# Kernel optimization log

Measured on AMD Instinct MI355X. Metric: run time of the kernel, lower is better.

The kernel has to match this reference:

```python
import jax, jax.numpy as jnp
import numpy as np

N = 4096        # num nodes
D = 512         # d_model (in_dim)
F = 512         # dff (out_dim)
H = 4           # num_heads
ALPHA = 0.3     # tf.keras LeakyReLU default


def setup_inputs() -> dict:
    key = jax.random.key(0)
    ks = jax.random.split(key, 9)
    s_in = 1.0 / np.sqrt(D)
    s_out = 1.0 / np.sqrt(F)
    return {
        "nodes": jax.random.normal(ks[0], (N, D), jnp.float32),
        "edges": jax.random.normal(ks[1], (N, D), jnp.float32),
        "labels": jax.random.normal(ks[2], (N, D), jnp.float32),
        # edge_layer Dense(dff)
        "We": jax.random.normal(ks[3], (D, F), jnp.float32) * s_in,
        "be": jnp.zeros((F,), jnp.float32),
        # per-head kernels stacked on leading head axis
        "W": jax.random.normal(ks[4], (H, D, F), jnp.float32) * s_in,
        "b": jax.random.normal(ks[5], (H, F), jnp.float32) * 0.01,
        "u": jax.random.normal(ks[6], (H, F), jnp.float32) * s_out,  # attn_kernel_self (squeezed)
        "v": jax.random.normal(ks[7], (H, F), jnp.float32) * s_out,  # attn_kernel_neighs (squeezed)
    }


def reference(nodes, edges, labels, We, be, W, b, u, v):
    # edge projection shared across heads: Dense(edges + labels)
    e = (edges + labels) @ We + be                       # [N, F]
    # per-head node projection: features = nodes @ W_h + b_h
    feats = jnp.einsum('nd,hdf->hnf', nodes, W) + b[:, None, :]   # [H, N, F]
    # rank-1 additive attention scores
    a_self = jnp.einsum('hnf,hf->hn', feats, u)          # [H, N]
    a_neigh = jnp.einsum('hnf,hf->hn', feats, v)         # [H, N]
    feats = feats + e[None]                              # [H, N, F]
    scores = a_self[:, :, None] * a_neigh[:, None, :]    # [H, N, N] outer product
    scores = jnp.where(scores >= 0, scores, ALPHA * scores)  # LeakyReLU(0.3)
    attn = jax.nn.softmax(scores, axis=-1)               # [H, N, N]
    out = jnp.einsum('hnm,hmf->hnf', attn, feats)        # [H, N, F]
    return jax.nn.relu(out.mean(axis=0))                 # [N, F]
```

## Files before the change

kernel.cpp:

```cpp
#include <hip/hip_runtime.h>

#define NN 4096
#define DD 512
#define FF 512
#define HH 4
#define KK 1024

typedef _Float16 f16;
typedef f16 f16x8 __attribute__((ext_vector_type(8)));
typedef f16 f16x4 __attribute__((ext_vector_type(4)));
typedef float f32x4 __attribute__((ext_vector_type(4)));
typedef float f32x16 __attribute__((ext_vector_type(16)));

typedef __attribute__((address_space(1))) void gvoid;
typedef __attribute__((address_space(3))) void svoid;
__device__ __forceinline__ void glds16(const void* g, void* s) {
    __builtin_amdgcn_global_load_lds((gvoid*)g, (svoid*)s, 16, 0, 0);
}

__device__ __attribute__((aligned(16))) f16 g_catA[NN * KK];
__device__ __attribute__((aligned(16))) f16 g_catB[HH * FF * KK];
__device__ __attribute__((aligned(16))) f16 g_featsH[HH * FF * NN];
__device__ __attribute__((aligned(16))) f16 g_oaccH[(size_t)2 * HH * NN * FF];
__device__ float g_Zp[2 * HH * NN];
__device__ float g_bcat[HH * FF];
__device__ float g_tu[HH * DD], g_tv[HH * DD], g_bu[HH], g_bv[HH];
__device__ float g_p[HH * NN], g_q[HH * NN], g_M[HH * NN];

#define PREP_CONV 4104
#define PREP_TRAN 320
#define PREP_UV   513

__global__ __launch_bounds__(256) void k_prep(const float* __restrict__ nodes, const float* __restrict__ edges,
                                              const float* __restrict__ labels, const float* __restrict__ We,
                                              const float* __restrict__ W, const float* __restrict__ be,
                                              const float* __restrict__ b, const float* __restrict__ u,
                                              const float* __restrict__ v) {
    __shared__ float lds[64 * 65];
    int bx = blockIdx.x;
    int tid = threadIdx.x;
    if (bx < PREP_CONV) {
        int id = bx * 256 + tid;
        const int NQ = NN * DD / 4;
        if (id < NQ) {
            f32x4 vv = *(const f32x4*)(nodes + (size_t)id * 4);
            f16x4 ov;
#pragma unroll
            for (int k = 0; k < 4; ++k) ov[k] = (f16)vv[k];
            *(f16x4*)&g_catA[(size_t)(id >> 7) * KK + (id & 127) * 4] = ov;
            return;
        }
        id -= NQ;
        if (id < NQ) {
            f32x4 ev = *(const f32x4*)(edges  + (size_t)id * 4);
            f32x4 lv = *(const f32x4*)(labels + (size_t)id * 4);
            f16x4 ov;
#pragma unroll
            for (int k = 0; k < 4; ++k) ov[k] = (f16)(ev[k] + lv[k]);
            *(f16x4*)&g_catA[(size_t)(id >> 7) * KK + 512 + (id & 127) * 4] = ov;
            return;
        }
        id -= NQ;
        if (id < HH * FF) { g_bcat[id] = b[id] + be[id & 511]; return; }
        return;
    }
    if (bx < PREP_CONV + PREP_TRAN) {
        int bid = bx - PREP_CONV;
        int mi = bid >> 6;
        int t64 = bid & 63;
        const float* src = (mi == 0) ? We : (W + (size_t)(mi - 1) * DD * FF);
        int ti = t64 >> 3, tj = t64 & 7;
        int r = tid >> 2, cseg = (tid & 3) * 16;
#pragma unroll
        for (int kq = 0; kq < 4; ++kq) {
            f32x4 vv = *(const f32x4*)(src + (size_t)(ti * 64 + r) * 512 + tj * 64 + cseg + kq * 4);
            *(f32x4*)&lds[r * 65 + cseg + kq * 4] = vv;
        }
        __syncthreads();
        int fl = tid >> 2, dseg = (tid & 3) * 16;
        f16x8 o0, o1;
#pragma unroll
        for (int k = 0; k < 8; ++k) o0[k] = (f16)lds[(dseg + k) * 65 + fl];
#pragma unroll
        for (int k = 0; k < 8; ++k) o1[k] = (f16)lds[(dseg + 8 + k) * 65 + fl];
        size_t frow = (size_t)(tj * 64 + fl);
        size_t dcol = (size_t)(ti * 64 + dseg);
        if (mi == 0) {
#pragma unroll
            for (int hh = 0; hh < HH; ++hh) {
                size_t ob = ((size_t)hh * FF + frow) * KK + 512 + dcol;
                *(f16x8*)&g_catB[ob] = o0;
                *(f16x8*)&g_catB[ob + 8] = o1;
            }
        } else {
            size_t ob = ((size_t)(mi - 1) * FF + frow) * KK + dcol;
            *(f16x8*)&g_catB[ob] = o0;
            *(f16x8*)&g_catB[ob + 8] = o1;
        }
        return;
    }
    {
        int row = (bx - PREP_CONV - PREP_TRAN) * 4 + (tid >> 6);
        int lane = tid & 63;
        float su = 0.f, sv = 0.f;
        if (row < HH * DD) {
            int h = row >> 9, d = row & 511;
            size_t wb = (size_t)h * DD * FF + (size_t)d * FF;
#pragma unroll
            for (int j = 0; j < 8; ++j) {
                int f = lane + 64 * j;
                float wv = W[wb + f];
                su += wv * u[(size_t)h * FF + f];
                sv += wv * v[(size_t)h * FF + f];
            }
        } else if (row < HH * DD + HH) {
            int h = row - HH * DD;
#pragma unroll
            for (int j = 0; j < 8; ++j) {
                int f = lane + 64 * j;
                float bvv = b[(size_t)h * FF + f];
                su += bvv * u[(size_t)h * FF + f];
                sv += bvv * v[(size_t)h * FF + f];
            }
        }
#pragma unroll
        for (int m = 1; m < 64; m <<= 1) {
            su += __shfl_xor(su, m, 64);
            sv += __shfl_xor(sv, m, 64);
        }
        if (lane == 0 && row < HH * DD + HH) {
            if (row < HH * DD) { g_tu[row] = su; g_tv[row] = sv; }
            else { g_bu[row - HH * DD] = su; g_bv[row - HH * DD] = sv; }
        }
    }
}

__global__ __launch_bounds__(256) void k_pq() {
    int row = blockIdx.x * 4 + (threadIdx.x >> 6);
    int lane = threadIdx.x & 63;
    int h = row >> 12, n = row & 4095;
    const f16* nb = g_catA + (size_t)n * KK + lane * 8;
    const float* tu = g_tu + h * DD + lane * 8;
    const float* tv = g_tv + h * DD + lane * 8;
    f16x8 nv8 = *(const f16x8*)nb;
    f32x4 tu0 = *(const f32x4*)tu, tu1 = *(const f32x4*)(tu + 4);
    f32x4 tv0 = *(const f32x4*)tv, tv1 = *(const f32x4*)(tv + 4);
    float pa = 0.f, qa = 0.f;
#pragma unroll
    for (int j = 0; j < 4; ++j) {
        float nv = (float)nv8[j];
        pa += nv * tu0[j];
        qa += nv * tv0[j];
    }
#pragma unroll
    for (int j = 0; j < 4; ++j) {
        float nv = (float)nv8[4 + j];
        pa += nv * tu1[j];
        qa += nv * tv1[j];
    }
#pragma unroll
    for (int m = 1; m < 64; m <<= 1) {
        pa += __shfl_xor(pa, m, 64);
        qa += __shfl_xor(qa, m, 64);
    }
    if (lane == 0) {
        g_p[row] = pa + g_bu[h];
        g_q[row] = qa + g_bv[h];
    }
}

__global__ __launch_bounds__(256, 2) void k_gemm_feats() {
    __shared__ f16 As[128 * 128];
    __shared__ f16 Bs[128 * 128];
    int tid = threadIdx.x;
    int lane = tid & 63, wave = tid >> 6;
    int wr = wave & 1, wc = wave >> 1;
    int c = lane & 15, g = lane >> 4;
    int n0 = blockIdx.x * 128, f0 = blockIdx.y * 128;
    int h = blockIdx.z;
    const f16* Bgl = g_catB + (size_t)h * FF * KK;
    int r4 = lane >> 4;
    int ch = lane & 15;
    f32x4 acc[4][4] = {};
    for (int kk = 0; kk < KK; kk += 128) {
        __syncthreads();
#pragma unroll
        for (int j = 0; j < 8; ++j) {
            int rowb = wave * 32 + j * 4;
            int row = rowb + r4;
            int src = (ch ^ (row & 15)) * 8;
            glds16(g_catA + (size_t)(n0 + row) * KK + kk + src, &As[rowb * 128]);
            glds16(Bgl    + (size_t)(f0 + row) * KK + kk + src, &Bs[rowb * 128]);
        }
        __syncthreads();
#pragma unroll
        for (int s = 0; s < 4; ++s) {
            f16x8 af[4], bf[4];
#pragma unroll
            for (int i = 0; i < 4; ++i) {
                int ra = wr * 64 + i * 16 + c;
                af[i] = *(const f16x8*)&As[ra * 128 + (((s * 4 + g) ^ (ra & 15)) * 8)];
            }
#pragma unroll
            for (int jj = 0; jj < 4; ++jj) {
                int rb = wc * 64 + jj * 16 + c;
                bf[jj] = *(const f16x8*)&Bs[rb * 128 + (((s * 4 + g) ^ (rb & 15)) * 8)];
            }
#pragma unroll
            for (int i = 0; i < 4; ++i)
#pragma unroll
                for (int jj = 0; jj < 4; ++jj)
                    acc[i][jj] = __builtin_amdgcn_mfma_f32_16x16x32_f16(af[i], bf[jj], acc[i][jj], 0, 0, 0);
        }
    }
#pragma unroll
    for (int jj = 0; jj < 4; ++jj) {
        int f = f0 + wc * 64 + jj * 16 + c;
        float bv = g_bcat[h * FF + f];
#pragma unroll
        for (int i = 0; i < 4; ++i) {
            int r0 = n0 + wr * 64 + i * 16 + g * 4;
            f16x4 ov;
#pragma unroll
            for (int rr = 0; rr < 4; ++rr) ov[rr] = (f16)(acc[i][jj][rr] + bv);
            *(f16x4*)(g_featsH + ((size_t)h * FF + f) * NN + r0) = ov;
        }
    }
}

__global__ __launch_bounds__(256) void k_mstat() {
    __shared__ float red[256];
    int h = blockIdx.x;
    int tid = threadIdx.x;
    float lmax = -1e30f, lmin = 1e30f;
    for (int i = tid; i < NN; i += 256) {
        float qv = g_q[h * NN + i];
        lmax = fmaxf(lmax, qv);
        lmin = fminf(lmin, qv);
    }
    red[tid] = lmax;
    __syncthreads();
    for (int s = 128; s > 0; s >>= 1) {
        if (tid < s) red[tid] = fmaxf(red[tid], red[tid + s]);
        __syncthreads();
    }
    float qmax = red[0];
    __syncthreads();
    red[tid] = lmin;
    __syncthreads();
    for (int s = 128; s > 0; s >>= 1) {
        if (tid < s) red[tid] = fminf(red[tid], red[tid + s]);
        __syncthreads();
    }
    float qmin = red[0];
#pragma unroll
    for (int j = 0; j < 16; ++j) {
        int n = tid + j * 256;
        float pv = g_p[h * NN + n];
        float se = pv * (pv >= 0.f ? qmax : qmin);
        g_M[h * NN + n] = fmaxf(se, 0.3f * se);
    }
}

#define WCALC(qv, dstvec, idx)                                              \
    {                                                                       \
        float s_ = pv * (qv);                                               \
        s_ = fmaxf(s_, 0.3f * s_);                                          \
        float e_ = __builtin_amdgcn_exp2f(__builtin_fmaf(s_, L2E, -mvb));   \
        zacc += e_;                                                         \
        dstvec[idx] = (f16)e_;                                              \
    }
#define GEN8(qa, qb, w)                                                     \
    {                                                                       \
        _Pragma("unroll") for (int k_ = 0; k_ < 4; ++k_) {                  \
            WCALC((qa)[k_], w, k_);                                         \
            WCALC((qb)[k_], w, 4 + k_);                                     \
        }                                                                   \
    }
#define STAGE_B(buf, kkoff)                                                 \
    {                                                                       \
        _Pragma("unroll") for (int j = 0; j < 8; ++j) {                     \
            int row_ = wave * 64 + j * 8 + r8;                              \
            glds16(Bgl + (size_t)row_ * NN + (kkoff) + ((ch ^ (row_ & 7)) * 8), \
                   &Bs[buf][(wave * 64 + j * 8) * 64]);                     \
        }                                                                   \
    }

__global__ __launch_bounds__(512, 2) void k_gemm_out() {
    __shared__ f16 As2[2][128 * 64];
    __shared__ f16 Bs[2][512 * 64];
    int tid = threadIdx.x;
    int lane = tid & 63, wave = tid >> 6;
    int wr = wave & 1;
    int wf = wave >> 1;
    int c5 = lane & 31, h5 = lane >> 5;
    int n0 = blockIdx.x * 128;
    int h = blockIdx.y;
    int ks = blockIdx.z;
    int wn = tid >> 2, kq = (tid & 3) * 16;
    const float L2E = 1.44269504f;
    float pv = g_p[h * NN + n0 + wn];
    float mvb = g_M[h * NN + n0 + wn] * L2E + 6.0f;
    const float* qh = g_q + h * NN + ks * 2048;
    const f16* Bgl = g_featsH + (size_t)h * FF * NN + (size_t)ks * 2048;
    int r8 = lane >> 3, ch = lane & 7;
    int aw0 = wn * 64 + (((tid & 3) * 2 + 0) ^ (wn & 7)) * 8;
    int aw1 = wn * 64 + (((tid & 3) * 2 + 1) ^ (wn & 7)) * 8;
    int arow = (wr * 64 + c5) * 64;
    int brow = (wf * 128 + c5) * 64;
    int csw = (c5 & 7);
    float zacc = 0.f;
    f32x16 acc[2][4] = {};
    f16x8 wA, wB;

    {
        const float* qp = qh + kq;
        f32x4 q0 = *(const f32x4*)qp, q1 = *(const f32x4*)(qp + 4),
              q2 = *(const f32x4*)(qp + 8), q3 = *(const f32x4*)(qp + 12);
        GEN8(q0, q1, wA);
        GEN8(q2, q3, wB);
        *(f16x8*)&As2[0][aw0] = wA;
        *(f16x8*)&As2[0][aw1] = wB;
        STAGE_B(0, 0);
        const float* qp1 = qh + 64 + kq;
        q0 = *(const f32x4*)qp1; q1 = *(const f32x4*)(qp1 + 4);
        q2 = *(const f32x4*)(qp1 + 8); q3 = *(const f32x4*)(qp1 + 12);
        GEN8(q0, q1, wA);
        GEN8(q2, q3, wB);
    }
    __syncthreads();

    int cur = 0;
    for (int t = 0; t < 32; ++t) {
        f32x4 q0, q1, q2, q3;
        if (t < 30) {
            const float* qp = qh + t * 64 + 128 + kq;
            q0 = *(const f32x4*)qp; q1 = *(const f32x4*)(qp + 4);
            q2 = *(const f32x4*)(qp + 8); q3 = *(const f32x4*)(qp + 12);
        }
        if (t < 31) {
            int nxt = cur ^ 1;
            int kk2 = t * 64 + 64;
            STAGE_B(nxt, kk2);
            *(f16x8*)&As2[nxt][aw0] = wA;
            *(f16x8*)&As2[nxt][aw1] = wB;
        }
#pragma unroll
        for (int sk = 0; sk < 4; ++sk) {
            int cph = ((sk * 2 + h5) ^ csw) * 8;
            f16x8 af0 = *(const f16x8*)&As2[cur][arow + cph];
            f16x8 af1 = *(const f16x8*)&As2[cur][arow + 2048 + cph];
            f16x8 bf0 = *(const f16x8*)&Bs[cur][brow + cph];
            f16x8 bf1 = *(const f16x8*)&Bs[cur][brow + 2048 + cph];
            f16x8 bf2 = *(const f16x8*)&Bs[cur][brow + 4096 + cph];
            f16x8 bf3 = *(const f16x8*)&Bs[cur][brow + 6144 + cph];
            acc[0][0] = __builtin_amdgcn_mfma_f32_32x32x16_f16(af0, bf0, acc[0][0], 0, 0, 0);
            acc[0][1] = __builtin_amdgcn_mfma_f32_32x32x16_f16(af0, bf1, acc[0][1], 0, 0, 0);
            acc[0][2] = __builtin_amdgcn_mfma_f32_32x32x16_f16(af0, bf2, acc[0][2], 0, 0, 0);
            acc[0][3] = __builtin_amdgcn_mfma_f32_32x32x16_f16(af0, bf3, acc[0][3], 0, 0, 0);
            acc[1][0] = __builtin_amdgcn_mfma_f32_32x32x16_f16(af1, bf0, acc[1][0], 0, 0, 0);
            acc[1][1] = __builtin_amdgcn_mfma_f32_32x32x16_f16(af1, bf1, acc[1][1], 0, 0, 0);
            acc[1][2] = __builtin_amdgcn_mfma_f32_32x32x16_f16(af1, bf2, acc[1][2], 0, 0, 0);
            acc[1][3] = __builtin_amdgcn_mfma_f32_32x32x16_f16(af1, bf3, acc[1][3], 0, 0, 0);
            if (t < 30) {
                if (sk == 1) GEN8(q0, q1, wA);
                if (sk == 2) GEN8(q2, q3, wB);
            }
        }
        __syncthreads();
        cur ^= 1;
    }
    zacc += __shfl_xor(zacc, 1, 64);
    zacc += __shfl_xor(zacc, 2, 64);
    if ((tid & 3) == 0) g_Zp[(size_t)(h * 2 + ks) * NN + n0 + wn] = zacc;
    f16* O = g_oaccH + (size_t)(h * 2 + ks) * NN * FF;
#pragma unroll
    for (int it = 0; it < 2; ++it)
#pragma unroll
        for (int jt = 0; jt < 4; ++jt) {
            int f = wf * 128 + jt * 32 + c5;
#pragma unroll
            for (int q = 0; q < 4; ++q) {
                int r0 = n0 + wr * 64 + it * 32 + q * 8 + h5 * 4;
#pragma unroll
                for (int rr = 0; rr < 4; ++rr)
                    O[(size_t)(r0 + rr) * FF + f] = (f16)acc[it][jt][q * 4 + rr];
            }
        }
}

__global__ void k_reduce(float* __restrict__ out) {
    int t = blockIdx.x * 256 + threadIdx.x;
    size_t i = (size_t)t * 8;
    int n = t >> 6;
    const size_t NF = (size_t)NN * FF;
    float s[8] = {0.f, 0.f, 0.f, 0.f, 0.f, 0.f, 0.f, 0.f};
#pragma unroll
    for (int h = 0; h < HH; ++h) {
        float Z = g_Zp[(size_t)(2 * h) * NN + n] + g_Zp[(size_t)(2 * h + 1) * NN + n];
        float sc = 0.25f / Z;
        f16x8 a = *(const f16x8*)(g_oaccH + (size_t)(2 * h) * NF + i);
        f16x8 bsl = *(const f16x8*)(g_oaccH + (size_t)(2 * h + 1) * NF + i);
#pragma unroll
        for (int rr = 0; rr < 8; ++rr) s[rr] += ((float)a[rr] + (float)bsl[rr]) * sc;
    }
    f32x4 o0, o1;
#pragma unroll
    for (int rr = 0; rr < 4; ++rr) o0[rr] = fmaxf(s[rr], 0.f);
#pragma unroll
    for (int rr = 0; rr < 4; ++rr) o1[rr] = fmaxf(s[4 + rr], 0.f);
    *(f32x4*)(out + i) = o0;
    *(f32x4*)(out + i + 4) = o1;
}

extern "C" void kernel_launch(void* const* d_in, const int* in_sizes, int n_in,
                              void* d_out, int out_size, void* d_ws, size_t ws_size,
                              hipStream_t stream) {
    (void)in_sizes; (void)n_in; (void)out_size; (void)d_ws; (void)ws_size;
    const float* nodes  = (const float*)d_in[0];
    const float* edges  = (const float*)d_in[1];
    const float* labels = (const float*)d_in[2];
    const float* We     = (const float*)d_in[3];
    const float* be     = (const float*)d_in[4];
    const float* W      = (const float*)d_in[5];
    const float* b      = (const float*)d_in[6];
    const float* u      = (const float*)d_in[7];
    const float* v      = (const float*)d_in[8];

    k_prep<<<PREP_CONV + PREP_TRAN + PREP_UV, 256, 0, stream>>>(nodes, edges, labels, We, W, be, b, u, v);
    k_pq<<<4096, 256, 0, stream>>>();
    k_gemm_feats<<<dim3(32, 4, 4), 256, 0, stream>>>();
    k_mstat<<<HH, 256, 0, stream>>>();
    k_gemm_out<<<dim3(32, 4, 2), 512, 0, stream>>>();
    k_reduce<<<1024, 256, 0, stream>>>((float*)d_out);
}
```

Measured before the change: 223.6 us.

## Split output GEMM over feature halves with smaller K tiles and MFMA priority

Splits the attention-output GEMM across two feature halves per block, doubling the grid to 512 blocks of 256 threads, and halves the K tile to 32 with padded A rows and a 4-way swizzle for B. It also raises wave priority around MFMA groups. The aim is better CU occupancy and less LDS per block, at the cost of recomputing the exp weights twice per row and doubling the number of loop iterations and barriers.

```diff
diff --git a/kernel.cpp b/kernel.cpp
--- a/kernel.cpp
+++ b/kernel.cpp
@@ -277,38 +277,39 @@
             WCALC((qb)[k_], w, 4 + k_);                                     \
         }                                                                   \
     }
-#define STAGE_B(buf, kkoff)                                                 \
+#define STAGE_B32(buf, mo)                                                  \
     {                                                                       \
-        _Pragma("unroll") for (int j = 0; j < 8; ++j) {                     \
-            int row_ = wave * 64 + j * 8 + r8;                              \
-            glds16(Bgl + (size_t)row_ * NN + (kkoff) + ((ch ^ (row_ & 7)) * 8), \
-                   &Bs[buf][(wave * 64 + j * 8) * 64]);                     \
+        _Pragma("unroll") for (int j_ = 0; j_ < 4; ++j_) {                  \
+            int rb_ = wave * 64 + j_ * 16;                                  \
+            glds16(Bgl + (size_t)(rb_ + srow) * NN + (mo) + ssrc,           \
+                   &Bs[buf][rb_ * 32]);                                     \
         }                                                                   \
     }
 
-__global__ __launch_bounds__(512, 2) void k_gemm_out() {
-    __shared__ f16 As2[2][128 * 64];
-    __shared__ f16 Bs[2][512 * 64];
+__global__ __launch_bounds__(256, 2) void k_gemm_out() {
+    __shared__ f16 As2[2][128 * 40];
+    __shared__ f16 Bs[2][256 * 32];
     int tid = threadIdx.x;
     int lane = tid & 63, wave = tid >> 6;
     int wr = wave & 1;
     int wf = wave >> 1;
     int c5 = lane & 31, h5 = lane >> 5;
     int n0 = blockIdx.x * 128;
-    int h = blockIdx.y;
-    int ks = blockIdx.z;
-    int wn = tid >> 2, kq = (tid & 3) * 16;
+    int fb = blockIdx.y * 256;
+    int h = blockIdx.z >> 1;
+    int ks = blockIdx.z & 1;
+    int wn = tid >> 1, kq = (tid & 1) * 16;
     const float L2E = 1.44269504f;
     float pv = g_p[h * NN + n0 + wn];
     float mvb = g_M[h * NN + n0 + wn] * L2E + 6.0f;
     const float* qh = g_q + h * NN + ks * 2048;
-    const f16* Bgl = g_featsH + (size_t)h * FF * NN + (size_t)ks * 2048;
-    int r8 = lane >> 3, ch = lane & 7;
-    int aw0 = wn * 64 + (((tid & 3) * 2 + 0) ^ (wn & 7)) * 8;
-    int aw1 = wn * 64 + (((tid & 3) * 2 + 1) ^ (wn & 7)) * 8;
-    int arow = (wr * 64 + c5) * 64;
-    int brow = (wf * 128 + c5) * 64;
-    int csw = (c5 & 7);
+    const f16* Bgl = g_featsH + ((size_t)h * FF + fb) * NN + (size_t)ks * 2048;
+    int srow = lane >> 2;
+    int ssrc = ((lane & 3) ^ (srow & 3)) * 8;
+    int aw = wn * 40 + kq;
+    int arow0 = (wr * 64 + c5) * 40;
+    int brow0 = (wf * 128 + c5) * 32;
+    int bxor = c5 & 3;
     float zacc = 0.f;
     f32x16 acc[2][4] = {};
     f16x8 wA, wB;
@@ -319,10 +320,10 @@
               q2 = *(const f32x4*)(qp + 8), q3 = *(const f32x4*)(qp + 12);
         GEN8(q0, q1, wA);
         GEN8(q2, q3, wB);
-        *(f16x8*)&As2[0][aw0] = wA;
-        *(f16x8*)&As2[0][aw1] = wB;
-        STAGE_B(0, 0);
-        const float* qp1 = qh + 64 + kq;
+        *(f16x8*)&As2[0][aw] = wA;
+        *(f16x8*)&As2[0][aw + 8] = wB;
+        STAGE_B32(0, 0);
+        const float* qp1 = qh + 32 + kq;
         q0 = *(const f32x4*)qp1; q1 = *(const f32x4*)(qp1 + 4);
         q2 = *(const f32x4*)(qp1 + 8); q3 = *(const f32x4*)(qp1 + 12);
         GEN8(q0, q1, wA);
@@ -331,29 +332,30 @@
     __syncthreads();
 
     int cur = 0;
-    for (int t = 0; t < 32; ++t) {
+    for (int t = 0; t < 64; ++t) {
         f32x4 q0, q1, q2, q3;
-        if (t < 30) {
-            const float* qp = qh + t * 64 + 128 + kq;
+        if (t < 62) {
+            const float* qp = qh + t * 32 + 64 + kq;
             q0 = *(const f32x4*)qp; q1 = *(const f32x4*)(qp + 4);
             q2 = *(const f32x4*)(qp + 8); q3 = *(const f32x4*)(qp + 12);
         }
-        if (t < 31) {
+        if (t < 63) {
             int nxt = cur ^ 1;
-            int kk2 = t * 64 + 64;
-            STAGE_B(nxt, kk2);
-            *(f16x8*)&As2[nxt][aw0] = wA;
-            *(f16x8*)&As2[nxt][aw1] = wB;
-        }
-#pragma unroll
-        for (int sk = 0; sk < 4; ++sk) {
-            int cph = ((sk * 2 + h5) ^ csw) * 8;
-            f16x8 af0 = *(const f16x8*)&As2[cur][arow + cph];
-            f16x8 af1 = *(const f16x8*)&As2[cur][arow + 2048 + cph];
-            f16x8 bf0 = *(const f16x8*)&Bs[cur][brow + cph];
-            f16x8 bf1 = *(const f16x8*)&Bs[cur][brow + 2048 + cph];
-            f16x8 bf2 = *(const f16x8*)&Bs[cur][brow + 4096 + cph];
-            f16x8 bf3 = *(const f16x8*)&Bs[cur][brow + 6144 + cph];
+            STAGE_B32(nxt, t * 32 + 32);
+            *(f16x8*)&As2[nxt][aw] = wA;
+            *(f16x8*)&As2[nxt][aw + 8] = wB;
+        }
+#pragma unroll
+        for (int sk = 0; sk < 2; ++sk) {
+            int cA = sk * 2 + h5;
+            f16x8 af0 = *(const f16x8*)&As2[cur][arow0 + cA * 8];
+            f16x8 af1 = *(const f16x8*)&As2[cur][arow0 + 32 * 40 + cA * 8];
+            int cB = (cA ^ bxor) * 8;
+            f16x8 bf0 = *(const f16x8*)&Bs[cur][brow0 + cB];
+            f16x8 bf1 = *(const f16x8*)&Bs[cur][brow0 + 1024 + cB];
+            f16x8 bf2 = *(const f16x8*)&Bs[cur][brow0 + 2048 + cB];
+            f16x8 bf3 = *(const f16x8*)&Bs[cur][brow0 + 3072 + cB];
+            __builtin_amdgcn_s_setprio(1);
             acc[0][0] = __builtin_amdgcn_mfma_f32_32x32x16_f16(af0, bf0, acc[0][0], 0, 0, 0);
             acc[0][1] = __builtin_amdgcn_mfma_f32_32x32x16_f16(af0, bf1, acc[0][1], 0, 0, 0);
             acc[0][2] = __builtin_amdgcn_mfma_f32_32x32x16_f16(af0, bf2, acc[0][2], 0, 0, 0);
@@ -362,23 +364,23 @@
             acc[1][1] = __builtin_amdgcn_mfma_f32_32x32x16_f16(af1, bf1, acc[1][1], 0, 0, 0);
             acc[1][2] = __builtin_amdgcn_mfma_f32_32x32x16_f16(af1, bf2, acc[1][2], 0, 0, 0);
             acc[1][3] = __builtin_amdgcn_mfma_f32_32x32x16_f16(af1, bf3, acc[1][3], 0, 0, 0);
-            if (t < 30) {
-                if (sk == 1) GEN8(q0, q1, wA);
-                if (sk == 2) GEN8(q2, q3, wB);
+            __builtin_amdgcn_s_setprio(0);
+            if (t < 62) {
+                if (sk == 0) { GEN8(q0, q1, wA); }
+                else         { GEN8(q2, q3, wB); }
             }
         }
         __syncthreads();
         cur ^= 1;
     }
     zacc += __shfl_xor(zacc, 1, 64);
-    zacc += __shfl_xor(zacc, 2, 64);
-    if ((tid & 3) == 0) g_Zp[(size_t)(h * 2 + ks) * NN + n0 + wn] = zacc;
+    if ((tid & 1) == 0) g_Zp[(size_t)(h * 2 + ks) * NN + n0 + wn] = zacc;
     f16* O = g_oaccH + (size_t)(h * 2 + ks) * NN * FF;
 #pragma unroll
     for (int it = 0; it < 2; ++it)
 #pragma unroll
         for (int jt = 0; jt < 4; ++jt) {
-            int f = wf * 128 + jt * 32 + c5;
+            int f = fb + wf * 128 + jt * 32 + c5;
 #pragma unroll
             for (int q = 0; q < 4; ++q) {
                 int r0 = n0 + wr * 64 + it * 32 + q * 8 + h5 * 4;
@@ -431,6 +433,6 @@
     k_pq<<<4096, 256, 0, stream>>>();
     k_gemm_feats<<<dim3(32, 4, 4), 256, 0, stream>>>();
     k_mstat<<<HH, 256, 0, stream>>>();
-    k_gemm_out<<<dim3(32, 4, 2), 512, 0, stream>>>();
+    k_gemm_out<<<dim3(32, 2, 8), 256, 0, stream>>>();
     k_reduce<<<1024, 256, 0, stream>>>((float*)d_out);
 }
```

Measured after the change: 240.3 us. 7.5% more time.

## Fuse max-stat into attention GEMM, load B directly to registers, XCD-aware grid

Applied to the files above, without the earlier changes.

Removes the separate k_mstat kernel and computes the per-head q max/min inside k_gemm_out with wave shuffles and a small LDS reduction. The B operand (featsH) is no longer staged through LDS with global_load_lds; each wave loads its own B fragments straight from global memory into registers, and the A tile uses a padded (68-stride) LDS layout instead of an XOR swizzle. The grid is flattened to 256 blocks so that consecutive block IDs map (head, k-split) onto XCDs for L2 locality, and warp tiling changes to 4x2 accumulators per wave. This cuts one launch and LDS traffic, at the cost of uncoalesced and unshared direct global B loads with less latency hiding.

```diff
diff --git a/kernel.cpp b/kernel.cpp
--- a/kernel.cpp
+++ b/kernel.cpp
@@ -25,7 +25,7 @@
 __device__ float g_Zp[2 * HH * NN];
 __device__ float g_bcat[HH * FF];
 __device__ float g_tu[HH * DD], g_tv[HH * DD], g_bu[HH], g_bv[HH];
-__device__ float g_p[HH * NN], g_q[HH * NN], g_M[HH * NN];
+__device__ float g_p[HH * NN], g_q[HH * NN];
 
 #define PREP_CONV 4104
 #define PREP_TRAN 320
@@ -228,40 +228,6 @@
     }
 }
 
-__global__ __launch_bounds__(256) void k_mstat() {
-    __shared__ float red[256];
-    int h = blockIdx.x;
-    int tid = threadIdx.x;
-    float lmax = -1e30f, lmin = 1e30f;
-    for (int i = tid; i < NN; i += 256) {
-        float qv = g_q[h * NN + i];
-        lmax = fmaxf(lmax, qv);
-        lmin = fminf(lmin, qv);
-    }
-    red[tid] = lmax;
-    __syncthreads();
-    for (int s = 128; s > 0; s >>= 1) {
-        if (tid < s) red[tid] = fmaxf(red[tid], red[tid + s]);
-        __syncthreads();
-    }
-    float qmax = red[0];
-    __syncthreads();
-    red[tid] = lmin;
-    __syncthreads();
-    for (int s = 128; s > 0; s >>= 1) {
-        if (tid < s) red[tid] = fminf(red[tid], red[tid + s]);
-        __syncthreads();
-    }
-    float qmin = red[0];
-#pragma unroll
-    for (int j = 0; j < 16; ++j) {
-        int n = tid + j * 256;
-        float pv = g_p[h * NN + n];
-        float se = pv * (pv >= 0.f ? qmax : qmin);
-        g_M[h * NN + n] = fmaxf(se, 0.3f * se);
-    }
-}
-
 #define WCALC(qv, dstvec, idx)                                              \
     {                                                                       \
         float s_ = pv * (qv);                                               \
@@ -277,40 +243,55 @@
             WCALC((qb)[k_], w, 4 + k_);                                     \
         }                                                                   \
     }
-#define STAGE_B(buf, kkoff)                                                 \
-    {                                                                       \
-        _Pragma("unroll") for (int j = 0; j < 8; ++j) {                     \
-            int row_ = wave * 64 + j * 8 + r8;                              \
-            glds16(Bgl + (size_t)row_ * NN + (kkoff) + ((ch ^ (row_ & 7)) * 8), \
-                   &Bs[buf][(wave * 64 + j * 8) * 64]);                     \
-        }                                                                   \
-    }
 
 __global__ __launch_bounds__(512, 2) void k_gemm_out() {
-    __shared__ f16 As2[2][128 * 64];
-    __shared__ f16 Bs[2][512 * 64];
+    __shared__ f16 As2[2][128 * 68];
+    __shared__ float redmax[8], redmin[8];
     int tid = threadIdx.x;
     int lane = tid & 63, wave = tid >> 6;
-    int wr = wave & 1;
-    int wf = wave >> 1;
+    int wf = wave;
     int c5 = lane & 31, h5 = lane >> 5;
-    int n0 = blockIdx.x * 128;
-    int h = blockIdx.y;
-    int ks = blockIdx.z;
+    int bid = blockIdx.x;
+    int xcd = bid & 7;
+    int h = xcd >> 1;
+    int ks = xcd & 1;
+    int n0 = (bid >> 3) * 128;
     int wn = tid >> 2, kq = (tid & 3) * 16;
     const float L2E = 1.44269504f;
     float pv = g_p[h * NN + n0 + wn];
-    float mvb = g_M[h * NN + n0 + wn] * L2E + 6.0f;
     const float* qh = g_q + h * NN + ks * 2048;
     const f16* Bgl = g_featsH + (size_t)h * FF * NN + (size_t)ks * 2048;
-    int r8 = lane >> 3, ch = lane & 7;
-    int aw0 = wn * 64 + (((tid & 3) * 2 + 0) ^ (wn & 7)) * 8;
-    int aw1 = wn * 64 + (((tid & 3) * 2 + 1) ^ (wn & 7)) * 8;
-    int arow = (wr * 64 + c5) * 64;
-    int brow = (wf * 128 + c5) * 64;
-    int csw = (c5 & 7);
+    float mvb;
+    {
+        const float* qfull = g_q + h * NN + tid * 8;
+        f32x4 a = *(const f32x4*)qfull, b2 = *(const f32x4*)(qfull + 4);
+        float lmax = -1e30f, lmin = 1e30f;
+#pragma unroll
+        for (int j = 0; j < 4; ++j) {
+            lmax = fmaxf(lmax, fmaxf(a[j], b2[j]));
+            lmin = fminf(lmin, fminf(a[j], b2[j]));
+        }
+#pragma unroll
+        for (int m = 1; m < 64; m <<= 1) {
+            lmax = fmaxf(lmax, __shfl_xor(lmax, m, 64));
+            lmin = fminf(lmin, __shfl_xor(lmin, m, 64));
+        }
+        if (lane == 0) { redmax[wave] = lmax; redmin[wave] = lmin; }
+        __syncthreads();
+        float qmax = redmax[0], qmin = redmin[0];
+#pragma unroll
+        for (int w2 = 1; w2 < 8; ++w2) {
+            qmax = fmaxf(qmax, redmax[w2]);
+            qmin = fminf(qmin, redmin[w2]);
+        }
+        float se = pv * (pv >= 0.f ? qmax : qmin);
+        float Mv = fmaxf(se, 0.3f * se);
+        mvb = Mv * L2E + 6.0f;
+    }
+    const f16* rowA = Bgl + (size_t)(wf * 64 + c5) * NN;
+    const f16* rowB = Bgl + (size_t)(wf * 64 + 32 + c5) * NN;
     float zacc = 0.f;
-    f32x16 acc[2][4] = {};
+    f32x16 acc[4][2] = {};
     f16x8 wA, wB;
 
     {
@@ -319,9 +300,8 @@
               q2 = *(const f32x4*)(qp + 8), q3 = *(const f32x4*)(qp + 12);
         GEN8(q0, q1, wA);
         GEN8(q2, q3, wB);
-        *(f16x8*)&As2[0][aw0] = wA;
-        *(f16x8*)&As2[0][aw1] = wB;
-        STAGE_B(0, 0);
+        *(f16x8*)&As2[0][wn * 68 + kq] = wA;
+        *(f16x8*)&As2[0][wn * 68 + kq + 8] = wB;
         const float* qp1 = qh + 64 + kq;
         q0 = *(const f32x4*)qp1; q1 = *(const f32x4*)(qp1 + 4);
         q2 = *(const f32x4*)(qp1 + 8); q3 = *(const f32x4*)(qp1 + 12);
@@ -332,39 +312,46 @@
 
     int cur = 0;
     for (int t = 0; t < 32; ++t) {
+        if (t < 31) {
+            int nxt = cur ^ 1;
+            *(f16x8*)&As2[nxt][wn * 68 + kq] = wA;
+            *(f16x8*)&As2[nxt][wn * 68 + kq + 8] = wB;
+        }
+        int mb = t * 64 + h5 * 8;
+        f16x8 b00 = *(const f16x8*)(rowA + mb);
+        f16x8 b01 = *(const f16x8*)(rowB + mb);
+        f16x8 b10 = *(const f16x8*)(rowA + mb + 16);
+        f16x8 b11 = *(const f16x8*)(rowB + mb + 16);
+        f16x8 b20 = *(const f16x8*)(rowA + mb + 32);
+        f16x8 b21 = *(const f16x8*)(rowB + mb + 32);
+        f16x8 b30 = *(const f16x8*)(rowA + mb + 48);
+        f16x8 b31 = *(const f16x8*)(rowB + mb + 48);
         f32x4 q0, q1, q2, q3;
         if (t < 30) {
             const float* qp = qh + t * 64 + 128 + kq;
             q0 = *(const f32x4*)qp; q1 = *(const f32x4*)(qp + 4);
             q2 = *(const f32x4*)(qp + 8); q3 = *(const f32x4*)(qp + 12);
         }
-        if (t < 31) {
-            int nxt = cur ^ 1;
-            int kk2 = t * 64 + 64;
-            STAGE_B(nxt, kk2);
-            *(f16x8*)&As2[nxt][aw0] = wA;
-            *(f16x8*)&As2[nxt][aw1] = wB;
-        }
 #pragma unroll
         for (int sk = 0; sk < 4; ++sk) {
-            int cph = ((sk * 2 + h5) ^ csw) * 8;
-            f16x8 af0 = *(const f16x8*)&As2[cur][arow + cph];
-            f16x8 af1 = *(const f16x8*)&As2[cur][arow + 2048 + cph];
-            f16x8 bf0 = *(const f16x8*)&Bs[cur][brow + cph];
-            f16x8 bf1 = *(const f16x8*)&Bs[cur][brow + 2048 + cph];
-            f16x8 bf2 = *(const f16x8*)&Bs[cur][brow + 4096 + cph];
-            f16x8 bf3 = *(const f16x8*)&Bs[cur][brow + 6144 + cph];
+            int cA = (sk * 2 + h5) * 8;
+            f16x8 af0 = *(const f16x8*)&As2[cur][(c5) * 68 + cA];
+            f16x8 af1 = *(const f16x8*)&As2[cur][(32 + c5) * 68 + cA];
+            f16x8 af2 = *(const f16x8*)&As2[cur][(64 + c5) * 68 + cA];
+            f16x8 af3 = *(const f16x8*)&As2[cur][(96 + c5) * 68 + cA];
+            f16x8 bf0 = (sk == 0) ? b00 : (sk == 1) ? b10 : (sk == 2) ? b20 : b30;
+            f16x8 bf1 = (sk == 0) ? b01 : (sk == 1) ? b11 : (sk == 2) ? b21 : b31;
             acc[0][0] = __builtin_amdgcn_mfma_f32_32x32x16_f16(af0, bf0, acc[0][0], 0, 0, 0);
             acc[0][1] = __builtin_amdgcn_mfma_f32_32x32x16_f16(af0, bf1, acc[0][1], 0, 0, 0);
-            acc[0][2] = __builtin_amdgcn_mfma_f32_32x32x16_f16(af0, bf2, acc[0][2], 0, 0, 0);
-            acc[0][3] = __builtin_amdgcn_mfma_f32_32x32x16_f16(af0, bf3, acc[0][3], 0, 0, 0);
             acc[1][0] = __builtin_amdgcn_mfma_f32_32x32x16_f16(af1, bf0, acc[1][0], 0, 0, 0);
             acc[1][1] = __builtin_amdgcn_mfma_f32_32x32x16_f16(af1, bf1, acc[1][1], 0, 0, 0);
-            acc[1][2] = __builtin_amdgcn_mfma_f32_32x32x16_f16(af1, bf2, acc[1][2], 0, 0, 0);
-            acc[1][3] = __builtin_amdgcn_mfma_f32_32x32x16_f16(af1, bf3, acc[1][3], 0, 0, 0);
+            acc[2][0] = __builtin_amdgcn_mfma_f32_32x32x16_f16(af2, bf0, acc[2][0], 0, 0, 0);
+            acc[2][1] = __builtin_amdgcn_mfma_f32_32x32x16_f16(af2, bf1, acc[2][1], 0, 0, 0);
+            acc[3][0] = __builtin_amdgcn_mfma_f32_32x32x16_f16(af3, bf0, acc[3][0], 0, 0, 0);
+            acc[3][1] = __builtin_amdgcn_mfma_f32_32x32x16_f16(af3, bf1, acc[3][1], 0, 0, 0);
             if (t < 30) {
-                if (sk == 1) GEN8(q0, q1, wA);
-                if (sk == 2) GEN8(q2, q3, wB);
+                if (sk == 1) { GEN8(q0, q1, wA); }
+                if (sk == 2) { GEN8(q2, q3, wB); }
             }
         }
         __syncthreads();
@@ -375,16 +362,16 @@
     if ((tid & 3) == 0) g_Zp[(size_t)(h * 2 + ks) * NN + n0 + wn] = zacc;
     f16* O = g_oaccH + (size_t)(h * 2 + ks) * NN * FF;
 #pragma unroll
-    for (int it = 0; it < 2; ++it)
-#pragma unroll
-        for (int jt = 0; jt < 4; ++jt) {
-            int f = wf * 128 + jt * 32 + c5;
-#pragma unroll
-            for (int q = 0; q < 4; ++q) {
-                int r0 = n0 + wr * 64 + it * 32 + q * 8 + h5 * 4;
+    for (int it = 0; it < 4; ++it)
+#pragma unroll
+        for (int jt = 0; jt < 2; ++jt) {
+            int f = wf * 64 + jt * 32 + c5;
+#pragma unroll
+            for (int qd = 0; qd < 4; ++qd) {
+                int r0 = n0 + it * 32 + qd * 8 + h5 * 4;
 #pragma unroll
                 for (int rr = 0; rr < 4; ++rr)
-                    O[(size_t)(r0 + rr) * FF + f] = (f16)acc[it][jt][q * 4 + rr];
+                    O[(size_t)(r0 + rr) * FF + f] = (f16)acc[it][jt][qd * 4 + rr];
             }
         }
 }
@@ -430,7 +417,6 @@
     k_prep<<<PREP_CONV + PREP_TRAN + PREP_UV, 256, 0, stream>>>(nodes, edges, labels, We, W, be, b, u, v);
     k_pq<<<4096, 256, 0, stream>>>();
     k_gemm_feats<<<dim3(32, 4, 4), 256, 0, stream>>>();
-    k_mstat<<<HH, 256, 0, stream>>>();
-    k_gemm_out<<<dim3(32, 4, 2), 512, 0, stream>>>();
+    k_gemm_out<<<256, 512, 0, stream>>>();
     k_reduce<<<1024, 256, 0, stream>>>((float*)d_out);
 }
```

New measurement: 224.4 us. About the same (+0.4%).

## Fuse max-stat pass into output GEMM and use 32x32 MFMA in feats GEMM

Applied to the files above, without the earlier changes.

Drops the separate k_mstat kernel. Each k_gemm_out block now computes the per-head q max and min itself with a wave-shuffle plus LDS reduction over all 4096 q values, then derives the softmax shift. This saves one launch and the global round trip of g_M, at the cost of every block redundantly reading and reducing the full q vector for its head. Separately, k_gemm_feats switches from 16x16x32 to 32x32x16 MFMA tiles, which means fewer LDS fragment loads per MFMA.

```diff
diff --git a/kernel.cpp b/kernel.cpp
--- a/kernel.cpp
+++ b/kernel.cpp
@@ -25,7 +25,7 @@
 __device__ float g_Zp[2 * HH * NN];
 __device__ float g_bcat[HH * FF];
 __device__ float g_tu[HH * DD], g_tv[HH * DD], g_bu[HH], g_bv[HH];
-__device__ float g_p[HH * NN], g_q[HH * NN], g_M[HH * NN];
+__device__ float g_p[HH * NN], g_q[HH * NN];
 
 #define PREP_CONV 4104
 #define PREP_TRAN 320
@@ -175,13 +175,15 @@
     int tid = threadIdx.x;
     int lane = tid & 63, wave = tid >> 6;
     int wr = wave & 1, wc = wave >> 1;
-    int c = lane & 15, g = lane >> 4;
+    int c5 = lane & 31, h5 = lane >> 5;
     int n0 = blockIdx.x * 128, f0 = blockIdx.y * 128;
     int h = blockIdx.z;
     const f16* Bgl = g_catB + (size_t)h * FF * KK;
     int r4 = lane >> 4;
     int ch = lane & 15;
-    f32x4 acc[4][4] = {};
+    f32x16 acc[2][2] = {};
+    int ra0 = wr * 64 + c5, ra1 = ra0 + 32;
+    int rb0 = wc * 64 + c5, rb1 = rb0 + 32;
     for (int kk = 0; kk < KK; kk += 128) {
         __syncthreads();
 #pragma unroll
@@ -194,72 +196,33 @@
         }
         __syncthreads();
 #pragma unroll
-        for (int s = 0; s < 4; ++s) {
-            f16x8 af[4], bf[4];
-#pragma unroll
-            for (int i = 0; i < 4; ++i) {
-                int ra = wr * 64 + i * 16 + c;
-                af[i] = *(const f16x8*)&As[ra * 128 + (((s * 4 + g) ^ (ra & 15)) * 8)];
-            }
-#pragma unroll
-            for (int jj = 0; jj < 4; ++jj) {
-                int rb = wc * 64 + jj * 16 + c;
-                bf[jj] = *(const f16x8*)&Bs[rb * 128 + (((s * 4 + g) ^ (rb & 15)) * 8)];
-            }
-#pragma unroll
-            for (int i = 0; i < 4; ++i)
-#pragma unroll
-                for (int jj = 0; jj < 4; ++jj)
-                    acc[i][jj] = __builtin_amdgcn_mfma_f32_16x16x32_f16(af[i], bf[jj], acc[i][jj], 0, 0, 0);
-        }
-    }
-#pragma unroll
-    for (int jj = 0; jj < 4; ++jj) {
-        int f = f0 + wc * 64 + jj * 16 + c;
-        float bv = g_bcat[h * FF + f];
-#pragma unroll
-        for (int i = 0; i < 4; ++i) {
-            int r0 = n0 + wr * 64 + i * 16 + g * 4;
-            f16x4 ov;
-#pragma unroll
-            for (int rr = 0; rr < 4; ++rr) ov[rr] = (f16)(acc[i][jj][rr] + bv);
-            *(f16x4*)(g_featsH + ((size_t)h * FF + f) * NN + r0) = ov;
-        }
-    }
-}
-
-__global__ __launch_bounds__(256) void k_mstat() {
-    __shared__ float red[256];
-    int h = blockIdx.x;
-    int tid = threadIdx.x;
-    float lmax = -1e30f, lmin = 1e30f;
-    for (int i = tid; i < NN; i += 256) {
-        float qv = g_q[h * NN + i];
-        lmax = fmaxf(lmax, qv);
-        lmin = fminf(lmin, qv);
-    }
-    red[tid] = lmax;
-    __syncthreads();
-    for (int s = 128; s > 0; s >>= 1) {
-        if (tid < s) red[tid] = fmaxf(red[tid], red[tid + s]);
-        __syncthreads();
-    }
-    float qmax = red[0];
-    __syncthreads();
-    red[tid] = lmin;
-    __syncthreads();
-    for (int s = 128; s > 0; s >>= 1) {
-        if (tid < s) red[tid] = fminf(red[tid], red[tid + s]);
-        __syncthreads();
-    }
-    float qmin = red[0];
-#pragma unroll
-    for (int j = 0; j < 16; ++j) {
-        int n = tid + j * 256;
-        float pv = g_p[h * NN + n];
-        float se = pv * (pv >= 0.f ? qmax : qmin);
-        g_M[h * NN + n] = fmaxf(se, 0.3f * se);
-    }
+        for (int sk = 0; sk < 8; ++sk) {
+            int lc = sk * 2 + h5;
+            f16x8 af0 = *(const f16x8*)&As[ra0 * 128 + ((lc ^ (ra0 & 15)) * 8)];
+            f16x8 af1 = *(const f16x8*)&As[ra1 * 128 + ((lc ^ (ra1 & 15)) * 8)];
+            f16x8 bf0 = *(const f16x8*)&Bs[rb0 * 128 + ((lc ^ (rb0 & 15)) * 8)];
+            f16x8 bf1 = *(const f16x8*)&Bs[rb1 * 128 + ((lc ^ (rb1 & 15)) * 8)];
+            acc[0][0] = __builtin_amdgcn_mfma_f32_32x32x16_f16(af0, bf0, acc[0][0], 0, 0, 0);
+            acc[0][1] = __builtin_amdgcn_mfma_f32_32x32x16_f16(af0, bf1, acc[0][1], 0, 0, 0);
+            acc[1][0] = __builtin_amdgcn_mfma_f32_32x32x16_f16(af1, bf0, acc[1][0], 0, 0, 0);
+            acc[1][1] = __builtin_amdgcn_mfma_f32_32x32x16_f16(af1, bf1, acc[1][1], 0, 0, 0);
+        }
+    }
+#pragma unroll
+    for (int it = 0; it < 2; ++it)
+#pragma unroll
+        for (int jt = 0; jt < 2; ++jt) {
+            int f = f0 + wc * 64 + jt * 32 + c5;
+            float bv = g_bcat[h * FF + f];
+#pragma unroll
+            for (int qd = 0; qd < 4; ++qd) {
+                int r0 = n0 + wr * 64 + it * 32 + qd * 8 + h5 * 4;
+                f16x4 ov;
+#pragma unroll
+                for (int rr = 0; rr < 4; ++rr) ov[rr] = (f16)(acc[it][jt][qd * 4 + rr] + bv);
+                *(f16x4*)(g_featsH + ((size_t)h * FF + f) * NN + r0) = ov;
+            }
+        }
 }
 
 #define WCALC(qv, dstvec, idx)                                              \
@@ -300,10 +263,38 @@
     int wn = tid >> 2, kq = (tid & 3) * 16;
     const float L2E = 1.44269504f;
     float pv = g_p[h * NN + n0 + wn];
-    float mvb = g_M[h * NN + n0 + wn] * L2E + 6.0f;
     const float* qh = g_q + h * NN + ks * 2048;
     const f16* Bgl = g_featsH + (size_t)h * FF * NN + (size_t)ks * 2048;
     int r8 = lane >> 3, ch = lane & 7;
+    float mvb;
+    {
+        const float* qfull = g_q + h * NN + tid * 8;
+        f32x4 a = *(const f32x4*)qfull, b2 = *(const f32x4*)(qfull + 4);
+        float lmax = -1e30f, lmin = 1e30f;
+#pragma unroll
+        for (int j = 0; j < 4; ++j) {
+            lmax = fmaxf(lmax, fmaxf(a[j], b2[j]));
+            lmin = fminf(lmin, fminf(a[j], b2[j]));
+        }
+#pragma unroll
+        for (int m = 1; m < 64; m <<= 1) {
+            lmax = fmaxf(lmax, __shfl_xor(lmax, m, 64));
+            lmin = fminf(lmin, __shfl_xor(lmin, m, 64));
+        }
+        float* red = (float*)&As2[0][0];
+        if (lane == 0) { red[wave] = lmax; red[8 + wave] = lmin; }
+        __syncthreads();
+        float qmax = red[0], qmin = red[8];
+#pragma unroll
+        for (int w2 = 1; w2 < 8; ++w2) {
+            qmax = fmaxf(qmax, red[w2]);
+            qmin = fminf(qmin, red[8 + w2]);
+        }
+        float se = pv * (pv >= 0.f ? qmax : qmin);
+        float Mv = fmaxf(se, 0.3f * se);
+        mvb = Mv * L2E + 6.0f;
+        __syncthreads();
+    }
     int aw0 = wn * 64 + (((tid & 3) * 2 + 0) ^ (wn & 7)) * 8;
     int aw1 = wn * 64 + (((tid & 3) * 2 + 1) ^ (wn & 7)) * 8;
     int arow = (wr * 64 + c5) * 64;
@@ -363,8 +354,8 @@
             acc[1][2] = __builtin_amdgcn_mfma_f32_32x32x16_f16(af1, bf2, acc[1][2], 0, 0, 0);
             acc[1][3] = __builtin_amdgcn_mfma_f32_32x32x16_f16(af1, bf3, acc[1][3], 0, 0, 0);
             if (t < 30) {
-                if (sk == 1) GEN8(q0, q1, wA);
-                if (sk == 2) GEN8(q2, q3, wB);
+                if (sk == 1) { GEN8(q0, q1, wA); }
+                if (sk == 2) { GEN8(q2, q3, wB); }
             }
         }
         __syncthreads();
@@ -380,11 +371,11 @@
         for (int jt = 0; jt < 4; ++jt) {
             int f = wf * 128 + jt * 32 + c5;
 #pragma unroll
-            for (int q = 0; q < 4; ++q) {
-                int r0 = n0 + wr * 64 + it * 32 + q * 8 + h5 * 4;
+            for (int qd = 0; qd < 4; ++qd) {
+                int r0 = n0 + wr * 64 + it * 32 + qd * 8 + h5 * 4;
 #pragma unroll
                 for (int rr = 0; rr < 4; ++rr)
-                    O[(size_t)(r0 + rr) * FF + f] = (f16)acc[it][jt][q * 4 + rr];
+                    O[(size_t)(r0 + rr) * FF + f] = (f16)acc[it][jt][qd * 4 + rr];
             }
         }
 }
@@ -430,7 +421,6 @@
     k_prep<<<PREP_CONV + PREP_TRAN + PREP_UV, 256, 0, stream>>>(nodes, edges, labels, We, W, be, b, u, v);
     k_pq<<<4096, 256, 0, stream>>>();
     k_gemm_feats<<<dim3(32, 4, 4), 256, 0, stream>>>();
-    k_mstat<<<HH, 256, 0, stream>>>();
     k_gemm_out<<<dim3(32, 4, 2), 512, 0, stream>>>();
     k_reduce<<<1024, 256, 0, stream>>>((float*)d_out);
 }
```

Measured after the change: 216.6 us. -3.1%, faster.
